# Kernel optimization log

Hardware: AMD Instinct MI355X
Metric: run time of the kernel (lower is better)

## Reference

```python
import jax, jax.numpy as jnp
import numpy as np
from jax import lax

BN_EPS = 1e-5

def _binarize(t):
    # deterministic sign binarization (sign(0)=0, matching torch.sign)
    return jnp.sign(t)

def setup_inputs() -> dict:
    key = jax.random.key(0)
    k1, k2 = jax.random.split(key)
    N, C, H, W = 16, 128, 128, 128
    x = jax.random.normal(k1, (N, C, H, W), dtype=jnp.float32)
    weight = jax.random.normal(k2, (C, C, 3, 3), dtype=jnp.float32)  # OIHW
    gamma = jnp.ones((C,), dtype=jnp.float32)
    beta = jnp.zeros((C,), dtype=jnp.float32)
    return {"x": x, "weight": weight, "gamma": gamma, "beta": beta}

def reference(x, weight, gamma, beta):
    residual = x
    # binarize activations (C != 3 path) and weights
    bx = _binarize(x)
    bw = _binarize(weight)
    # 3x3 conv, stride 1, padding 1, no bias
    out = lax.conv_general_dilated(
        bx, bw,
        window_strides=(1, 1),
        padding=((1, 1), (1, 1)),
        dimension_numbers=("NCHW", "OIHW", "NCHW"),
    )
    # BatchNorm2d in training mode: batch stats over (N, H, W), biased variance
    mean = jnp.mean(out, axis=(0, 2, 3))
    var = jnp.var(out, axis=(0, 2, 3))
    inv = lax.rsqrt(var + BN_EPS)
    out = (out - mean[None, :, None, None]) * (inv * gamma)[None, :, None, None] + beta[None, :, None, None]
    # Hardtanh
    out = jnp.clip(out, -1.0, 1.0)
    return out + residual
```

## Files before the change

### kernel.cpp

```cpp
#include <hip/hip_runtime.h>
#include <stdint.h>

#define Nn 16
#define Cc 128
#define Hh 128
#define Ww 128
#define HWc (Hh*Ww)
#define NHW 262144

#define PIXB 132
#define ROWP 17408
#define NROW 130

typedef int v4i  __attribute__((ext_vector_type(4)));
typedef int v16i __attribute__((ext_vector_type(16)));

typedef __attribute__((address_space(3))) unsigned int lds_uint;
typedef __attribute__((address_space(1))) const unsigned int glob_uint;

__device__ __forceinline__ void gload_lds16(const void* g, void* l) {
    __builtin_amdgcn_global_load_lds((glob_uint*)g, (lds_uint*)l, 16, 0, 0);
}

__global__ __launch_bounds__(256) void pack_x(const float* __restrict__ x,
                                              char* __restrict__ x8) {
    int bid = blockIdx.x;
    int n = bid / NROW, r = bid % NROW;
    char* row = x8 + (size_t)bid * ROWP;
    int t = threadIdx.x;

    if (r == 0 || r == NROW - 1) {
        for (int i = t; i < ROWP / 16; i += 256)
            ((uint4*)row)[i] = make_uint4(0, 0, 0, 0);
        return;
    }
    int h = r - 1;
    if (t < 33)                ((uint32_t*)row)[t] = 0;
    else if (t >= 64 && t < 97) ((uint32_t*)(row + 129 * PIXB))[t - 64] = 0;

    __shared__ char tile[128 * PIXB];
    const float* px = x + (((size_t)n * Cc) * Hh + h) * Ww;
    int w = t & 127, ch = t >> 7;
    for (int q = 0; q < 16; ++q) {
        int c = ch * 64 + q * 4;
        uint32_t d = 0;
        #pragma unroll
        for (int j = 0; j < 4; ++j) {
            float v = px[(size_t)(c + j) * HWc + w];
            int8_t s = (v > 0.f) ? 1 : ((v < 0.f) ? -1 : 0);
            d |= (uint32_t)(uint8_t)s << (8 * j);
        }
        *(uint32_t*)(tile + w * PIXB + c) = d;
    }
    __syncthreads();
    for (int s = 0; s < 4; ++s) {
        int idx = s * 256 + t;
        int ww = idx >> 3, cb = idx & 7;
        const uint32_t* src = (const uint32_t*)(tile + ww * PIXB + cb * 16);
        uint32_t* dst = (uint32_t*)(row + (1 + ww) * PIXB + cb * 16);
        dst[0] = src[0]; dst[1] = src[1]; dst[2] = src[2]; dst[3] = src[3];
    }
}

__global__ __launch_bounds__(256) void pack_w(const float* __restrict__ wt,
                                              char* __restrict__ wswz) {
    int gid = blockIdx.x * 256 + threadIdx.x;
    if (gid >= 9216) return;
    int lane = gid & 63, grp = gid >> 6;
    int kh = grp & 3, tap = (grp >> 2) % 9, ot = grp / 36;
    int o  = ot * 32 + (lane & 31);
    int cb = kh * 32 + (lane >> 5) * 16;
    uint32_t dw4[4];
    #pragma unroll
    for (int di = 0; di < 4; ++di) {
        uint32_t d = 0;
        #pragma unroll
        for (int j = 0; j < 4; ++j) {
            int c = cb + di * 4 + j;
            float v = wt[((size_t)o * Cc + c) * 9 + tap];
            int8_t s = (v > 0.f) ? 1 : ((v < 0.f) ? -1 : 0);
            d |= (uint32_t)(uint8_t)s << (8 * j);
        }
        dw4[di] = d;
    }
    *(uint4*)(wswz + (size_t)gid * 16) = make_uint4(dw4[0], dw4[1], dw4[2], dw4[3]);
}

template <typename OutT>
__global__ __launch_bounds__(256) void conv_mfma2(const char* __restrict__ x8,
                                                  const char* __restrict__ wswz,
                                                  OutT* __restrict__ out) {
    __shared__ char lds[3 * ROWP];
    int bid = blockIdx.x;
    int n = bid >> 7, h = bid & 127;
    int tid = threadIdx.x, lane = tid & 63, wid = tid >> 6;

    const char* gbase = x8 + ((size_t)n * NROW + h) * ROWP;
    for (int task = wid; task < 51; task += 4) {
        int rr = task / 17, ck = task % 17;
        gload_lds16(gbase + (size_t)rr * ROWP + ck * 1024 + lane * 16,
                    lds + rr * ROWP + ck * 1024);
    }
    __syncthreads();

    int wy = wid >> 1, wx = wid & 1;
    int ln31 = lane & 31, lq = lane >> 5;

    v16i acc[2][2];
    #pragma unroll
    for (int oi = 0; oi < 2; ++oi)
        #pragma unroll
        for (int pi = 0; pi < 2; ++pi)
            #pragma unroll
            for (int r2 = 0; r2 < 16; ++r2) acc[oi][pi][r2] = 0;

    const char* wb0 = wswz + (size_t)(wy * 2 * 9) * 4096 + lane * 16;
    const char* lb  = lds + (1 + wx * 64 + ln31) * PIXB + lq * 16;

    #pragma unroll
    for (int tap = 0; tap < 9; ++tap) {
        int rr = tap / 3, dw = tap % 3 - 1;
        #pragma unroll
        for (int kh = 0; kh < 4; ++kh) {
            v4i a0 = *(const v4i*)(wb0 + (tap * 4 + kh) * 1024);
            v4i a1 = *(const v4i*)(wb0 + (36 + tap * 4 + kh) * 1024);
            const uint32_t* p0 = (const uint32_t*)(lb + rr * ROWP + dw * PIXB + kh * 32);
            const uint32_t* p1 = p0 + (32 * PIXB) / 4;
            v4i b0, b1;
            #pragma unroll
            for (int j = 0; j < 4; ++j) { b0[j] = (int)p0[j]; b1[j] = (int)p1[j]; }
            acc[0][0] = __builtin_amdgcn_mfma_i32_32x32x32_i8(a0, b0, acc[0][0], 0, 0, 0);
            acc[0][1] = __builtin_amdgcn_mfma_i32_32x32x32_i8(a0, b1, acc[0][1], 0, 0, 0);
            acc[1][0] = __builtin_amdgcn_mfma_i32_32x32x32_i8(a1, b0, acc[1][0], 0, 0, 0);
            acc[1][1] = __builtin_amdgcn_mfma_i32_32x32x32_i8(a1, b1, acc[1][1], 0, 0, 0);
        }
    }

    OutT* po = out + ((size_t)n * Cc) * HWc + (size_t)h * Ww;
    #pragma unroll
    for (int oi = 0; oi < 2; ++oi)
        #pragma unroll
        for (int pi = 0; pi < 2; ++pi) {
            int wcol = wx * 64 + pi * 32 + ln31;
            #pragma unroll
            for (int r2 = 0; r2 < 16; ++r2) {
                int orow = wy * 64 + oi * 32 + (r2 & 3) + 8 * (r2 >> 2) + 4 * lq;
                po[(size_t)orow * HWc + wcol] = (OutT)acc[oi][pi][r2];
            }
        }
}

__global__ __launch_bounds__(256) void stats16(const short* __restrict__ conv,
                                               unsigned long long* __restrict__ stats) {
    int b = blockIdx.x;
    int c = b & 127, n = b >> 7;
    const uint4* p = (const uint4*)(conv + (size_t)(n * Cc + c) * HWc);
    int sum = 0, sq = 0;
    for (int i = threadIdx.x; i < HWc / 8; i += 256) {
        uint4 v = p[i];
        uint32_t ua[4] = {v.x, v.y, v.z, v.w};
        #pragma unroll
        for (int j = 0; j < 4; ++j) {
            int s0 = (short)(ua[j] & 0xffff), s1 = (short)(ua[j] >> 16);
            sum += s0 + s1;
            sq  += s0 * s0 + s1 * s1;
        }
    }
    #pragma unroll
    for (int off = 32; off > 0; off >>= 1) {
        sum += __shfl_down(sum, off);
        sq  += __shfl_down(sq, off);
    }
    __shared__ int wsum[4], wsq[4];
    int wave = threadIdx.x >> 6, lane = threadIdx.x & 63;
    if (lane == 0) { wsum[wave] = sum; wsq[wave] = sq; }
    __syncthreads();
    if (threadIdx.x == 0) {
        long long S = 0, Q = 0;
        #pragma unroll
        for (int i = 0; i < 4; ++i) { S += wsum[i]; Q += wsq[i]; }
        atomicAdd(&stats[c],       (unsigned long long)S);
        atomicAdd(&stats[128 + c], (unsigned long long)Q);
    }
}

__global__ __launch_bounds__(256) void statsf(const float* __restrict__ conv,
                                              unsigned long long* __restrict__ stats) {
    int b = blockIdx.x;
    int c = b & 127, n = b >> 7;
    const float4* p = (const float4*)(conv + (size_t)(n * Cc + c) * HWc);
    int sum = 0, sq = 0;
    for (int i = threadIdx.x; i < HWc / 4; i += 256) {
        float4 v = p[i];
        int a = (int)v.x, d = (int)v.y, e = (int)v.z, f = (int)v.w;
        sum += a + d + e + f;
        sq  += a * a + d * d + e * e + f * f;
    }
    #pragma unroll
    for (int off = 32; off > 0; off >>= 1) {
        sum += __shfl_down(sum, off);
        sq  += __shfl_down(sq, off);
    }
    __shared__ int wsum[4], wsq[4];
    int wave = threadIdx.x >> 6, lane = threadIdx.x & 63;
    if (lane == 0) { wsum[wave] = sum; wsq[wave] = sq; }
    __syncthreads();
    if (threadIdx.x == 0) {
        long long S = 0, Q = 0;
        #pragma unroll
        for (int i = 0; i < 4; ++i) { S += wsum[i]; Q += wsq[i]; }
        atomicAdd(&stats[c],       (unsigned long long)S);
        atomicAdd(&stats[128 + c], (unsigned long long)Q);
    }
}

__device__ __forceinline__ void bn_coef(const unsigned long long* stats,
                                        const float* gamma, const float* beta,
                                        int c, float& scale, float& shift) {
    long long S = (long long)stats[c];
    long long Q = (long long)stats[128 + c];
    double m   = (double)S / (double)NHW;
    double var = (double)Q / (double)NHW - m * m;
    float inv  = (float)(1.0 / sqrt(var + 1e-5));
    scale = inv * gamma[c];
    shift = beta[c] - (float)m * scale;
}

__global__ __launch_bounds__(256) void apply16(float* __restrict__ out,
                                               const short* __restrict__ conv,
                                               const float* __restrict__ x,
                                               const unsigned long long* __restrict__ stats,
                                               const float* __restrict__ gamma,
                                               const float* __restrict__ beta) {
    int b = blockIdx.x;
    int c = b & 127, n = b >> 7;
    size_t basei = (size_t)(n * Cc + c) * HWc;
    float scale, shift;
    bn_coef(stats, gamma, beta, c, scale, shift);

    const uint4*  pc = (const uint4*)(conv + basei);
    const float4* px = (const float4*)(x + basei);
    float4*       po = (float4*)(out + basei);
    for (int i = threadIdx.x; i < HWc / 8; i += 256) {
        uint4 v = pc[i];
        uint32_t ua[4] = {v.x, v.y, v.z, v.w};
        #pragma unroll
        for (int half = 0; half < 2; ++half) {
            float4 r = px[i * 2 + half];
            float4 o;
            float c0 = (float)(short)(ua[half * 2]     & 0xffff);
            float c1 = (float)(short)(ua[half * 2]     >> 16);
            float c2 = (float)(short)(ua[half * 2 + 1] & 0xffff);
            float c3 = (float)(short)(ua[half * 2 + 1] >> 16);
            o.x = fminf(fmaxf(c0 * scale + shift, -1.0f), 1.0f) + r.x;
            o.y = fminf(fmaxf(c1 * scale + shift, -1.0f), 1.0f) + r.y;
            o.z = fminf(fmaxf(c2 * scale + shift, -1.0f), 1.0f) + r.z;
            o.w = fminf(fmaxf(c3 * scale + shift, -1.0f), 1.0f) + r.w;
            po[i * 2 + half] = o;
        }
    }
}

__global__ __launch_bounds__(256) void applyf(float* __restrict__ out,
                                              const float* __restrict__ x,
                                              const unsigned long long* __restrict__ stats,
                                              const float* __restrict__ gamma,
                                              const float* __restrict__ beta) {
    int b = blockIdx.x;
    int c = b & 127, n = b >> 7;
    size_t basei = (size_t)(n * Cc + c) * HWc;
    float scale, shift;
    bn_coef(stats, gamma, beta, c, scale, shift);

    float4* po = (float4*)(out + basei);
    const float4* px = (const float4*)(x + basei);
    for (int i = threadIdx.x; i < HWc / 4; i += 256) {
        float4 v = po[i];
        float4 r = px[i];
        v.x = fminf(fmaxf(v.x * scale + shift, -1.0f), 1.0f) + r.x;
        v.y = fminf(fmaxf(v.y * scale + shift, -1.0f), 1.0f) + r.y;
        v.z = fminf(fmaxf(v.z * scale + shift, -1.0f), 1.0f) + r.z;
        v.w = fminf(fmaxf(v.w * scale + shift, -1.0f), 1.0f) + r.w;
        po[i] = v;
    }
}

extern "C" void kernel_launch(void* const* d_in, const int* in_sizes, int n_in,
                              void* d_out, int out_size, void* d_ws, size_t ws_size,
                              hipStream_t stream) {
    const float* x     = (const float*)d_in[0];
    const float* wt    = (const float*)d_in[1];
    const float* gamma = (const float*)d_in[2];
    const float* beta  = (const float*)d_in[3];
    float* out = (float*)d_out;

    char* ws = (char*)d_ws;
    unsigned long long* stats = (unsigned long long*)ws;
    char* wswz = ws + 4096;
    char* x8   = ws + 262144;
    const size_t x8_bytes = (size_t)Nn * NROW * ROWP;
    short* conv16 = (short*)(ws + 262144 + x8_bytes);
    const size_t need16 = 262144 + x8_bytes + (size_t)NHW * Cc * 2;

    hipMemsetAsync(stats, 0, 2048, stream);
    pack_x<<<Nn * NROW, 256, 0, stream>>>(x, x8);
    pack_w<<<36, 256, 0, stream>>>(wt, wswz);

    if (ws_size >= need16) {
        conv_mfma2<short><<<Nn * Hh, 256, 0, stream>>>(x8, wswz, conv16);
        stats16<<<Nn * Cc, 256, 0, stream>>>(conv16, stats);
        apply16<<<Nn * Cc, 256, 0, stream>>>(out, conv16, x, stats, gamma, beta);
    } else {
        conv_mfma2<float><<<Nn * Hh, 256, 0, stream>>>(x8, wswz, out);
        statsf<<<Nn * Cc, 256, 0, stream>>>(out, stats);
        applyf<<<Nn * Cc, 256, 0, stream>>>(out, x, stats, gamma, beta);
    }
}
```

Baseline: 363.5 us.

## Use channel-group-major packed row layout for 16-byte LDS reads and swizzle blocks

Repacks each padded row from pixel-major (132-byte pixel stride) to 8 channel groups of 130 pixels × 16 bytes. The conv kernel can then read each B operand with a single 16-byte LDS load instead of four 4-byte loads. It also hoists all weight fragment loads for a tap ahead of the MFMAs, and remaps block indices so consecutive blocks land on different batch images. The intent is to cut LDS instruction count and bank conflicts and to improve scheduling, at some cost in register pressure and possible L2 locality changes.

```diff
diff --git a/kernel.cpp b/kernel.cpp
--- a/kernel.cpp
+++ b/kernel.cpp
@@ -8,9 +8,11 @@
 #define HWc (Hh*Ww)
 #define NHW 262144
 
-#define PIXB 132
 #define ROWP 17408
 #define NROW 130
+#define XGRP 2176
+
+#define PIXB 132
 
 typedef int v4i  __attribute__((ext_vector_type(4)));
 typedef int v16i __attribute__((ext_vector_type(16)));
@@ -35,8 +37,10 @@
         return;
     }
     int h = r - 1;
-    if (t < 33)                ((uint32_t*)row)[t] = 0;
-    else if (t >= 64 && t < 97) ((uint32_t*)(row + 129 * PIXB))[t - 64] = 0;
+    if (t < 16) {
+        int g = t >> 1, p = (t & 1) ? 129 : 0;
+        *(uint4*)(row + g * XGRP + p * 16) = make_uint4(0, 0, 0, 0);
+    }
 
     __shared__ char tile[128 * PIXB];
     const float* px = x + (((size_t)n * Cc) * Hh + h) * Ww;
@@ -55,9 +59,9 @@
     __syncthreads();
     for (int s = 0; s < 4; ++s) {
         int idx = s * 256 + t;
-        int ww = idx >> 3, cb = idx & 7;
-        const uint32_t* src = (const uint32_t*)(tile + ww * PIXB + cb * 16);
-        uint32_t* dst = (uint32_t*)(row + (1 + ww) * PIXB + cb * 16);
+        int w2 = idx & 127, g = idx >> 7;
+        const uint32_t* src = (const uint32_t*)(tile + w2 * PIXB + g * 16);
+        uint32_t* dst = (uint32_t*)(row + g * XGRP + (1 + w2) * 16);
         dst[0] = src[0]; dst[1] = src[1]; dst[2] = src[2]; dst[3] = src[3];
     }
 }
@@ -91,7 +95,8 @@
                                                   const char* __restrict__ wswz,
                                                   OutT* __restrict__ out) {
     __shared__ char lds[3 * ROWP];
-    int bid = blockIdx.x;
+    int bid0 = blockIdx.x;
+    int bid = (bid0 & 7) * 256 + (bid0 >> 3);
     int n = bid >> 7, h = bid & 127;
     int tid = threadIdx.x, lane = tid & 63, wid = tid >> 6;
 
@@ -115,24 +120,26 @@
             for (int r2 = 0; r2 < 16; ++r2) acc[oi][pi][r2] = 0;
 
     const char* wb0 = wswz + (size_t)(wy * 2 * 9) * 4096 + lane * 16;
-    const char* lb  = lds + (1 + wx * 64 + ln31) * PIXB + lq * 16;
+    const char* lb  = lds + (size_t)(1 + wx * 64 + ln31) * 16 + lq * XGRP;
 
     #pragma unroll
     for (int tap = 0; tap < 9; ++tap) {
         int rr = tap / 3, dw = tap % 3 - 1;
+        v4i a0[4], a1[4];
         #pragma unroll
         for (int kh = 0; kh < 4; ++kh) {
-            v4i a0 = *(const v4i*)(wb0 + (tap * 4 + kh) * 1024);
-            v4i a1 = *(const v4i*)(wb0 + (36 + tap * 4 + kh) * 1024);
-            const uint32_t* p0 = (const uint32_t*)(lb + rr * ROWP + dw * PIXB + kh * 32);
-            const uint32_t* p1 = p0 + (32 * PIXB) / 4;
-            v4i b0, b1;
-            #pragma unroll
-            for (int j = 0; j < 4; ++j) { b0[j] = (int)p0[j]; b1[j] = (int)p1[j]; }
-            acc[0][0] = __builtin_amdgcn_mfma_i32_32x32x32_i8(a0, b0, acc[0][0], 0, 0, 0);
-            acc[0][1] = __builtin_amdgcn_mfma_i32_32x32x32_i8(a0, b1, acc[0][1], 0, 0, 0);
-            acc[1][0] = __builtin_amdgcn_mfma_i32_32x32x32_i8(a1, b0, acc[1][0], 0, 0, 0);
-            acc[1][1] = __builtin_amdgcn_mfma_i32_32x32x32_i8(a1, b1, acc[1][1], 0, 0, 0);
+            a0[kh] = *(const v4i*)(wb0 + (tap * 4 + kh) * 1024);
+            a1[kh] = *(const v4i*)(wb0 + (36 + tap * 4 + kh) * 1024);
+        }
+        const char* pb = lb + rr * ROWP + dw * 16;
+        #pragma unroll
+        for (int kh = 0; kh < 4; ++kh) {
+            v4i b0 = *(const v4i*)(pb + kh * (2 * XGRP));
+            v4i b1 = *(const v4i*)(pb + kh * (2 * XGRP) + 512);
+            acc[0][0] = __builtin_amdgcn_mfma_i32_32x32x32_i8(a0[kh], b0, acc[0][0], 0, 0, 0);
+            acc[0][1] = __builtin_amdgcn_mfma_i32_32x32x32_i8(a0[kh], b1, acc[0][1], 0, 0, 0);
+            acc[1][0] = __builtin_amdgcn_mfma_i32_32x32x32_i8(a1[kh], b0, acc[1][0], 0, 0, 0);
+            acc[1][1] = __builtin_amdgcn_mfma_i32_32x32x32_i8(a1[kh], b1, acc[1][1], 0, 0, 0);
         }
     }
 
```

Measured after the change: 352.2 us. -3.1%, faster.
